# Kernel optimization log

Hardware: AMD Instinct MI355X
Metric: run time of the kernel (lower is better)

Reference implementation:

```python
import jax, jax.numpy as jnp
import numpy as np

B, S, E = 2, 2048, 1024
G, Q, D = 4, 4, 64          # n_groups, queries-per-group, head dim
SCALE = 1.0 / np.sqrt(E).astype(np.float32)  # sequence_attention=False -> 1/sqrt(embed_dim)


def setup_inputs() -> dict:
    key = jax.random.key(0)
    ks = jax.random.split(key, 12)
    init = lambda k, shp, fan_in: jax.random.uniform(k, shp, jnp.float32, -1.0, 1.0) / np.sqrt(fan_in)
    return {
        "q": jax.random.normal(ks[0], (B, S, E), jnp.float32),
        "k": jax.random.normal(ks[1], (B, S, E), jnp.float32),
        "v": jax.random.normal(ks[2], (B, S, E), jnp.float32),
        "Wq_w": init(ks[3], (E, G * Q * D), E),
        "Wq_b": init(ks[4], (G * Q * D,), E),
        "Wk_w": init(ks[5], (E, G * D), E),
        "Wk_b": init(ks[6], (G * D,), E),
        "Wv_w": init(ks[7], (E, G * D), E),
        "Wv_b": init(ks[8], (G * D,), E),
        "fc_w": init(ks[9], (G * Q * D, G * Q * D), G * Q * D),
        "fc_b": init(ks[10], (G * Q * D,), G * Q * D),
    }


def reference(q, k, v, Wq_w, Wq_b, Wk_w, Wk_b, Wv_w, Wv_b, fc_w, fc_b):
    # projections
    qh = (q @ Wq_w + Wq_b).reshape(B, S, G, Q, D)   # b s g q d
    kh = (k @ Wk_w + Wk_b).reshape(B, S, G, D)      # b s g d (1 KV head per group)
    vh = (v @ Wv_w + Wv_b).reshape(B, S, G, D)
    # energy: broadcast single KV head across Q query heads per group
    energy = jnp.einsum('bsgqd,btgd->bgqst', qh, kh) * SCALE  # [b,g,q,s,s]
    attn = jax.nn.softmax(energy, axis=-1)
    out = jnp.einsum('bgqst,btgd->bsgqd', attn, vh)           # b s g q d
    out = out.reshape(B, S, G * Q * D)                        # b s (g q d)
    return out @ fc_w + fc_b
```

## Files before the change

### kernel.cpp

```cpp
#include <hip/hip_runtime.h>


typedef unsigned short u16;
typedef __attribute__((ext_vector_type(4))) unsigned short u16x4;
typedef __attribute__((ext_vector_type(8))) short bf16x8;
typedef __attribute__((ext_vector_type(8))) unsigned short u16x8;
typedef __attribute__((ext_vector_type(4))) float f32x4;
typedef __attribute__((ext_vector_type(8))) float f32x8;

#define MFMA16(a, b, c) __builtin_amdgcn_mfma_f32_16x16x32_bf16(a, b, c, 0, 0, 0)
#define SC2L 0.045084140608f

__device__ __forceinline__ u16 f2b(float f) {
  unsigned int i = __builtin_bit_cast(unsigned int, f);
  i += 0x7fffu + ((i >> 16) & 1u);
  return (u16)(i >> 16);
}
__device__ __forceinline__ unsigned cvtpk_bf16(float a, float b) {
  unsigned r;
  asm("v_cvt_pk_bf16_f32 %0, %1, %2" : "=v"(r) : "v"(a), "v"(b));
  return r;
}
__device__ __forceinline__ void gload_lds16(const u16* g, u16* l) {
  __builtin_amdgcn_global_load_lds(
      (const __attribute__((address_space(1))) unsigned int*)g,
      (__attribute__((address_space(3))) unsigned int*)l, 16, 0, 0);
}

__global__ __launch_bounds__(256) void transpose_all(const float* __restrict__ Wq_w,
                                                     const float* __restrict__ Wk_w,
                                                     const float* __restrict__ Wv_w,
                                                     const float* __restrict__ fc_w,
                                                     u16* __restrict__ WqT,
                                                     u16* __restrict__ WkT,
                                                     u16* __restrict__ WvT,
                                                     u16* __restrict__ fcT) {
  __shared__ u16 tile[32][33];
  int r = blockIdx.x;
  const float* W; u16* Wt; int N; float scale;
  if (r < 1024)      { W = Wq_w; Wt = WqT; N = 1024; scale = SC2L; }
  else if (r < 1280) { W = Wk_w; Wt = WkT; N = 256;  scale = 1.0f; r -= 1024; }
  else if (r < 1536) { W = Wv_w; Wt = WvT; N = 256;  scale = 1.0f; r -= 1280; }
  else               { W = fc_w; Wt = fcT; N = 1024; scale = 1.0f; r -= 1536; }
  const int K = 1024;
  const int bk = (r & 31) * 32;
  const int bn = (r >> 5) * 32;
  const int tx = threadIdx.x & 31, ty = threadIdx.x >> 5;
#pragma unroll
  for (int rr = ty; rr < 32; rr += 8)
    tile[rr][tx] = f2b(W[(size_t)(bk + rr) * N + bn + tx] * scale);
  __syncthreads();
#pragma unroll
  for (int rr = ty; rr < 32; rr += 8) Wt[(size_t)(bn + rr) * K + bk + tx] = tile[tx][rr];
}

template <typename AT, typename CT>
__device__ __forceinline__ void gemm_body(const AT* __restrict__ A,
                                          const u16* __restrict__ Bt,
                                          const float* __restrict__ bias,
                                          CT* __restrict__ C,
                                          int M, int N, int K, float bscale,
                                          bool transv, int bid) {
  __shared__ alignas(16) u16 As[2][64 * 32];
  __shared__ alignas(16) u16 Bs[2][128 * 32];
  const int tid = threadIdx.x;
  const int lane = tid & 63, wave = tid >> 6;
  const int l15 = lane & 15, lg = lane >> 4;
  const int nb = N >> 7;
  const int bm = (bid / nb) << 6;
  const int bn = (bid % nb) << 7;
  const int wr = (wave >> 2) << 5;
  const int wc = (wave & 3) << 5;
  const int crow = tid >> 2;
  const int ccol = (tid & 3) * 8;
  const AT*  arow = A  + (size_t)(bm + crow) * K + ccol;
  const u16* brow = Bt + (size_t)(bn + crow) * K + ccol;

  f32x4 acc[2][2] = {};
  const int nt = K >> 5;

  if (tid < 256) {
    if constexpr (__is_same(AT, float)) {
      const f32x8 af0 = *(const f32x8*)(arow);
      u16x8 av; unsigned* aw = (unsigned*)&av;
#pragma unroll
      for (int j = 0; j < 4; ++j) aw[j] = cvtpk_bf16(af0[2 * j], af0[2 * j + 1]);
      *(u16x8*)(As[0] + tid * 8) = av;
    } else {
      gload_lds16(arow, As[0] + tid * 8);
    }
  }
  gload_lds16(brow, Bs[0] + tid * 8);
  __syncthreads();

#pragma unroll 2
  for (int t = 0; t < nt; ++t) {
    const int c = t & 1;
    const int k1 = (t + 1) << 5;
    f32x8 afn;
    if (t + 1 < nt) {
      if (tid < 256) {
        if constexpr (__is_same(AT, float)) {
          afn = *(const f32x8*)(arow + k1);
        } else {
          gload_lds16(arow + k1, As[c ^ 1] + tid * 8);
        }
      }
      gload_lds16(brow + k1, Bs[c ^ 1] + tid * 8);
    }

    bf16x8 af[2], bf[2];
#pragma unroll
    for (int m = 0; m < 2; ++m)
      af[m] = *(const bf16x8*)(As[c] + (wr + m * 16 + l15) * 32 + lg * 8);
#pragma unroll
    for (int n = 0; n < 2; ++n)
      bf[n] = *(const bf16x8*)(Bs[c] + (wc + n * 16 + l15) * 32 + lg * 8);
#pragma unroll
    for (int m = 0; m < 2; ++m)
#pragma unroll
      for (int n = 0; n < 2; ++n) acc[m][n] = MFMA16(af[m], bf[n], acc[m][n]);

    if constexpr (__is_same(AT, float)) {
      if (t + 1 < nt && tid < 256) {
        u16x8 av; unsigned* aw = (unsigned*)&av;
#pragma unroll
        for (int j = 0; j < 4; ++j) aw[j] = cvtpk_bf16(afn[2 * j], afn[2 * j + 1]);
        *(u16x8*)(As[c ^ 1] + tid * 8) = av;
      }
    }
    __syncthreads();
  }

  float bvv[2];
#pragma unroll
  for (int n = 0; n < 2; ++n) bvv[n] = bias[bn + wc + n * 16 + l15] * bscale;

  if (transv) {
#pragma unroll
    for (int m = 0; m < 2; ++m) {
      const int row = bm + wr + m * 16 + lg * 4;
      const int bb = row >> 11, t = row & 2047;
#pragma unroll
      for (int n = 0; n < 2; ++n) {
        const int col = bn + wc + n * 16 + l15;
        u16x4 pk;
#pragma unroll
        for (int rr = 0; rr < 4; ++rr) pk[rr] = f2b(acc[m][n][rr] + bvv[n]);
        *(u16x4*)(C + (size_t)bb * ((size_t)N * 2048) + (size_t)col * 2048 + t) = pk;
      }
    }
  } else {
#pragma unroll
    for (int m = 0; m < 2; ++m) {
      const int row = bm + wr + m * 16 + lg * 4;
#pragma unroll
      for (int rr = 0; rr < 4; ++rr) {
        CT* cp = C + (size_t)(row + rr) * N + bn + wc + l15;
#pragma unroll
        for (int n = 0; n < 2; ++n) {
          const float val = acc[m][n][rr] + bvv[n];
          if constexpr (__is_same(CT, u16)) cp[n * 16] = f2b(val);
          else                              cp[n * 16] = val;
        }
      }
    }
  }
}

__global__ __launch_bounds__(512, 4) void gemm_qkv(const float* __restrict__ q,
                                                   const float* __restrict__ k,
                                                   const float* __restrict__ v,
                                                   const u16* __restrict__ WqT,
                                                   const u16* __restrict__ WkT,
                                                   const u16* __restrict__ WvT,
                                                   const float* __restrict__ Wq_b,
                                                   const float* __restrict__ Wk_b,
                                                   const float* __restrict__ Wv_b,
                                                   u16* __restrict__ qh,
                                                   u16* __restrict__ kh,
                                                   u16* __restrict__ vt) {
  if (blockIdx.x < 512)
    gemm_body<float, u16>(q, WqT, Wq_b, qh, 4096, 1024, 1024, SC2L, false, blockIdx.x);
  else if (blockIdx.x < 640)
    gemm_body<float, u16>(k, WkT, Wk_b, kh, 4096, 256, 1024, 1.0f, false, blockIdx.x - 512);
  else
    gemm_body<float, u16>(v, WvT, Wv_b, vt, 4096, 256, 1024, 1.0f, true, blockIdx.x - 640);
}

template <typename AT, typename CT, bool TRANSV>
__global__ __launch_bounds__(512, 4) void gemm_bt_bias(const AT* __restrict__ A,
                                                       const u16* __restrict__ Bt,
                                                       const float* __restrict__ bias,
                                                       CT* __restrict__ C,
                                                       int M, int N, int K, float bscale) {
  gemm_body<AT, CT>(A, Bt, bias, C, M, N, K, bscale, TRANSV, blockIdx.x);
}

__global__ __launch_bounds__(512, 2) void attn_fwd(const u16* __restrict__ qh,
                                                   const u16* __restrict__ kh,
                                                   const u16* __restrict__ vhT,
                                                   u16* __restrict__ ao) {
  constexpr int S = 2048;
  __shared__ alignas(16) u16 Klds[2][128][72];
  __shared__ alignas(16) u16 Vt[2][64][136];

  const int tid = threadIdx.x;
  const int lane = tid & 63, w = tid >> 6;
  const int h = w & 3, ssub = w >> 2;
  const int l15 = lane & 15, lg = lane >> 4;
  const int bid = blockIdx.x;
  const int s0 = (bid & 31) << 6;
  const int g = (bid >> 5) & 3;
  const int b = bid >> 7;
  const int sbase = s0 + ssub * 32;

  bf16x8 qf[2][2];
#pragma unroll
  for (int sh = 0; sh < 2; ++sh) {
    const u16* qrow = qh + (((size_t)(b * S + sbase + sh * 16 + l15)) << 10)
                      + g * 256 + h * 64 + lg * 8;
    qf[sh][0] = *(const bf16x8*)(qrow);
    qf[sh][1] = *(const bf16x8*)(qrow + 32);
  }

  const u16* kbase = kh + (((size_t)(b * S)) << 8) + g * 64;
  const u16* vtbase = vhT + ((size_t)(b * 256 + g * 64)) * 2048;

  bf16x8 ones;
#pragma unroll
  for (int j = 0; j < 8; ++j) ones[j] = (short)0x3F80;

  f32x4 lacc[2] = {};
  f32x4 o[2][4] = {};

  const int srow = tid >> 3;
  const int sdp = (tid & 7) * 8;
  const int sig = (srow & 32) | (((srow >> 2) & 1) << 4) | (((srow >> 3) & 3) << 2) | (srow & 3);
  const int vrow = tid >> 4;
  const int vcol = (tid & 15) * 8;

  u16x8 kv[2], vv[2];
#define LOADTILE(T0)                                                                   \
  do {                                                                                 \
    kv[0] = *(const u16x8*)(kbase + (size_t)((T0) + srow) * 256 + sdp);                \
    kv[1] = *(const u16x8*)(kbase + (size_t)((T0) + 64 + srow) * 256 + sdp);           \
    vv[0] = *(const u16x8*)(vtbase + (size_t)vrow * 2048 + (T0) + vcol);               \
    vv[1] = *(const u16x8*)(vtbase + (size_t)(vrow + 32) * 2048 + (T0) + vcol);        \
  } while (0)

  LOADTILE(0);

#pragma unroll 2
  for (int i = 0; i < 16; ++i) {
    const int c = i & 1;
    *(u16x8*)(&Klds[c][sig][sdp])       = kv[0];
    *(u16x8*)(&Klds[c][sig + 64][sdp])  = kv[1];
    *(u16x8*)(&Vt[c][vrow][vcol])       = vv[0];
    *(u16x8*)(&Vt[c][vrow + 32][vcol])  = vv[1];
    __syncthreads();
    if (i + 1 < 16) LOADTILE((i + 1) << 7);

#pragma unroll
    for (int tti = 0; tti < 2; ++tti) {
      const int tt = tti ^ ssub;
#pragma unroll
      for (int kk = 0; kk < 2; ++kk) {
        float p[2][8];
#pragma unroll
        for (int nn = 0; nn < 2; ++nn) {
          const int n = kk * 2 + nn;
          const bf16x8 bk0 = *(const bf16x8*)(&Klds[c][tt * 64 + n * 16 + l15][lg * 8]);
          const bf16x8 bk1 = *(const bf16x8*)(&Klds[c][tt * 64 + n * 16 + l15][32 + lg * 8]);
          __builtin_amdgcn_s_setprio(1);
#pragma unroll
          for (int sh = 0; sh < 2; ++sh) {
            f32x4 z = {};
            z = MFMA16(bk0, qf[sh][0], z);
            z = MFMA16(bk1, qf[sh][1], z);
            __builtin_amdgcn_s_setprio(0);
#pragma unroll
            for (int r = 0; r < 4; ++r)
              p[sh][nn * 4 + r] = exp2f(z[r]);
          }
        }
        bf16x8 pa[2];
#pragma unroll
        for (int sh = 0; sh < 2; ++sh) {
          unsigned* paw = (unsigned*)&pa[sh];
          paw[0] = cvtpk_bf16(p[sh][0], p[sh][1]);
          paw[1] = cvtpk_bf16(p[sh][2], p[sh][3]);
          paw[2] = cvtpk_bf16(p[sh][4], p[sh][5]);
          paw[3] = cvtpk_bf16(p[sh][6], p[sh][7]);
        }
        __builtin_amdgcn_s_setprio(1);
        lacc[0] = MFMA16(pa[0], ones, lacc[0]);
        lacc[1] = MFMA16(pa[1], ones, lacc[1]);
#pragma unroll
        for (int nd = 0; nd < 4; ++nd) {
          const bf16x8 bv = *(const bf16x8*)(&Vt[c][nd * 16 + l15][tt * 64 + kk * 32 + lg * 8]);
          o[0][nd] = MFMA16(pa[0], bv, o[0][nd]);
          o[1][nd] = MFMA16(pa[1], bv, o[1][nd]);
        }
        __builtin_amdgcn_s_setprio(0);
      }
    }
  }
#undef LOADTILE

#pragma unroll
  for (int sh = 0; sh < 2; ++sh) {
#pragma unroll
    for (int r = 0; r < 4; ++r) {
      const float invr = 1.f / lacc[sh][r];
      u16* orow = ao + (((size_t)(b * S + sbase + sh * 16 + lg * 4 + r)) << 10)
                  + g * 256 + h * 64 + l15;
#pragma unroll
      for (int nd = 0; nd < 4; ++nd) orow[nd * 16] = f2b(o[sh][nd][r] * invr);
    }
  }
}

extern "C" void kernel_launch(void* const* d_in, const int* in_sizes, int n_in,
                              void* d_out, int out_size, void* d_ws, size_t ws_size,
                              hipStream_t stream) {
  const float* q    = (const float*)d_in[0];
  const float* k    = (const float*)d_in[1];
  const float* v    = (const float*)d_in[2];
  const float* Wq_w = (const float*)d_in[3];
  const float* Wq_b = (const float*)d_in[4];
  const float* Wk_w = (const float*)d_in[5];
  const float* Wk_b = (const float*)d_in[6];
  const float* Wv_w = (const float*)d_in[7];
  const float* Wv_b = (const float*)d_in[8];
  const float* fc_w = (const float*)d_in[9];
  const float* fc_b = (const float*)d_in[10];
  float* out = (float*)d_out;

  u16* ws  = (u16*)d_ws;
  u16* WqT = ws;
  u16* WkT = WqT + 1024 * 1024;
  u16* WvT = WkT + 256 * 1024;
  u16* fcT = WvT + 256 * 1024;
  u16* qhp = fcT + 1024 * 1024;
  u16* khp = qhp + 4096 * 1024;
  u16* vtp = khp + 4096 * 256;
  u16* aop = vtp + 4096 * 256;

  transpose_all<<<2560, 256, 0, stream>>>(Wq_w, Wk_w, Wv_w, fc_w, WqT, WkT, WvT, fcT);

  gemm_qkv<<<768, 512, 0, stream>>>(q, k, v, WqT, WkT, WvT, Wq_b, Wk_b, Wv_b,
                                    qhp, khp, vtp);

  attn_fwd<<<256, 512, 0, stream>>>(qhp, khp, vtp, aop);

  gemm_bt_bias<u16, float, false><<<512, 512, 0, stream>>>(aop, fcT, fc_b, out, 4096, 1024, 1024, 1.0f);
}
```

Before: 113.8 us.

## Widen GEMM per-wave tiles to 256 threads and double attention KV tile

```diff
diff --git a/kernel.cpp b/kernel.cpp
--- a/kernel.cpp
+++ b/kernel.cpp
@@ -69,28 +69,28 @@
   const int nb = N >> 7;
   const int bm = (bid / nb) << 6;
   const int bn = (bid % nb) << 7;
-  const int wr = (wave >> 2) << 5;
-  const int wc = (wave & 3) << 5;
+  const int wr = (wave >> 1) << 5;
+  const int wc = (wave & 1) << 6;
   const int crow = tid >> 2;
   const int ccol = (tid & 3) * 8;
-  const AT*  arow = A  + (size_t)(bm + crow) * K + ccol;
-  const u16* brow = Bt + (size_t)(bn + crow) * K + ccol;
-
-  f32x4 acc[2][2] = {};
+  const AT*  arow  = A  + (size_t)(bm + crow) * K + ccol;
+  const u16* brow0 = Bt + (size_t)(bn + crow) * K + ccol;
+  const u16* brow1 = Bt + (size_t)(bn + crow + 64) * K + ccol;
+
+  f32x4 acc[2][4] = {};
   const int nt = K >> 5;
 
-  if (tid < 256) {
-    if constexpr (__is_same(AT, float)) {
-      const f32x8 af0 = *(const f32x8*)(arow);
-      u16x8 av; unsigned* aw = (unsigned*)&av;
-#pragma unroll
-      for (int j = 0; j < 4; ++j) aw[j] = cvtpk_bf16(af0[2 * j], af0[2 * j + 1]);
-      *(u16x8*)(As[0] + tid * 8) = av;
-    } else {
-      gload_lds16(arow, As[0] + tid * 8);
-    }
-  }
-  gload_lds16(brow, Bs[0] + tid * 8);
+  if constexpr (__is_same(AT, float)) {
+    const f32x8 af0 = *(const f32x8*)(arow);
+    u16x8 av; unsigned* aw = (unsigned*)&av;
+#pragma unroll
+    for (int j = 0; j < 4; ++j) aw[j] = cvtpk_bf16(af0[2 * j], af0[2 * j + 1]);
+    *(u16x8*)(As[0] + tid * 8) = av;
+  } else {
+    gload_lds16(arow, As[0] + tid * 8);
+  }
+  gload_lds16(brow0, Bs[0] + tid * 8);
+  gload_lds16(brow1, Bs[0] + (tid + 256) * 8);
   __syncthreads();
 
 #pragma unroll 2
@@ -99,30 +99,29 @@
     const int k1 = (t + 1) << 5;
     f32x8 afn;
     if (t + 1 < nt) {
-      if (tid < 256) {
-        if constexpr (__is_same(AT, float)) {
-          afn = *(const f32x8*)(arow + k1);
-        } else {
-          gload_lds16(arow + k1, As[c ^ 1] + tid * 8);
-        }
-      }
-      gload_lds16(brow + k1, Bs[c ^ 1] + tid * 8);
-    }
-
-    bf16x8 af[2], bf[2];
+      if constexpr (__is_same(AT, float)) {
+        afn = *(const f32x8*)(arow + k1);
+      } else {
+        gload_lds16(arow + k1, As[c ^ 1] + tid * 8);
+      }
+      gload_lds16(brow0 + k1, Bs[c ^ 1] + tid * 8);
+      gload_lds16(brow1 + k1, Bs[c ^ 1] + (tid + 256) * 8);
+    }
+
+    bf16x8 af[2], bf[4];
 #pragma unroll
     for (int m = 0; m < 2; ++m)
       af[m] = *(const bf16x8*)(As[c] + (wr + m * 16 + l15) * 32 + lg * 8);
 #pragma unroll
-    for (int n = 0; n < 2; ++n)
+    for (int n = 0; n < 4; ++n)
       bf[n] = *(const bf16x8*)(Bs[c] + (wc + n * 16 + l15) * 32 + lg * 8);
 #pragma unroll
     for (int m = 0; m < 2; ++m)
 #pragma unroll
-      for (int n = 0; n < 2; ++n) acc[m][n] = MFMA16(af[m], bf[n], acc[m][n]);
+      for (int n = 0; n < 4; ++n) acc[m][n] = MFMA16(af[m], bf[n], acc[m][n]);
 
     if constexpr (__is_same(AT, float)) {
-      if (t + 1 < nt && tid < 256) {
+      if (t + 1 < nt) {
         u16x8 av; unsigned* aw = (unsigned*)&av;
 #pragma unroll
         for (int j = 0; j < 4; ++j) aw[j] = cvtpk_bf16(afn[2 * j], afn[2 * j + 1]);
@@ -132,9 +131,9 @@
     __syncthreads();
   }
 
-  float bvv[2];
-#pragma unroll
-  for (int n = 0; n < 2; ++n) bvv[n] = bias[bn + wc + n * 16 + l15] * bscale;
+  float bvv[4];
+#pragma unroll
+  for (int n = 0; n < 4; ++n) bvv[n] = bias[bn + wc + n * 16 + l15] * bscale;
 
   if (transv) {
 #pragma unroll
@@ -142,7 +141,7 @@
       const int row = bm + wr + m * 16 + lg * 4;
       const int bb = row >> 11, t = row & 2047;
 #pragma unroll
-      for (int n = 0; n < 2; ++n) {
+      for (int n = 0; n < 4; ++n) {
         const int col = bn + wc + n * 16 + l15;
         u16x4 pk;
 #pragma unroll
@@ -158,7 +157,7 @@
       for (int rr = 0; rr < 4; ++rr) {
         CT* cp = C + (size_t)(row + rr) * N + bn + wc + l15;
 #pragma unroll
-        for (int n = 0; n < 2; ++n) {
+        for (int n = 0; n < 4; ++n) {
           const float val = acc[m][n][rr] + bvv[n];
           if constexpr (__is_same(CT, u16)) cp[n * 16] = f2b(val);
           else                              cp[n * 16] = val;
@@ -168,7 +167,7 @@
   }
 }
 
-__global__ __launch_bounds__(512, 4) void gemm_qkv(const float* __restrict__ q,
+__global__ __launch_bounds__(256, 4) void gemm_qkv(const float* __restrict__ q,
                                                    const float* __restrict__ k,
                                                    const float* __restrict__ v,
                                                    const u16* __restrict__ WqT,
@@ -189,7 +188,7 @@
 }
 
 template <typename AT, typename CT, bool TRANSV>
-__global__ __launch_bounds__(512, 4) void gemm_bt_bias(const AT* __restrict__ A,
+__global__ __launch_bounds__(256, 4) void gemm_bt_bias(const AT* __restrict__ A,
                                                        const u16* __restrict__ Bt,
                                                        const float* __restrict__ bias,
                                                        CT* __restrict__ C,
@@ -202,8 +201,8 @@
                                                    const u16* __restrict__ vhT,
                                                    u16* __restrict__ ao) {
   constexpr int S = 2048;
-  __shared__ alignas(16) u16 Klds[2][128][72];
-  __shared__ alignas(16) u16 Vt[2][64][136];
+  __shared__ alignas(16) u16 Klds[2][256][72];
+  __shared__ alignas(16) u16 Vt[2][64][264];
 
   const int tid = threadIdx.x;
   const int lane = tid & 63, w = tid >> 6;
@@ -234,36 +233,38 @@
   f32x4 lacc[2] = {};
   f32x4 o[2][4] = {};
 
-  const int srow = tid >> 3;
-  const int sdp = (tid & 7) * 8;
-  const int sig = (srow & 32) | (((srow >> 2) & 1) << 4) | (((srow >> 3) & 3) << 2) | (srow & 3);
-  const int vrow = tid >> 4;
-  const int vcol = (tid & 15) * 8;
-
-  u16x8 kv[2], vv[2];
-#define LOADTILE(T0)                                                                   \
-  do {                                                                                 \
-    kv[0] = *(const u16x8*)(kbase + (size_t)((T0) + srow) * 256 + sdp);                \
-    kv[1] = *(const u16x8*)(kbase + (size_t)((T0) + 64 + srow) * 256 + sdp);           \
-    vv[0] = *(const u16x8*)(vtbase + (size_t)vrow * 2048 + (T0) + vcol);               \
-    vv[1] = *(const u16x8*)(vtbase + (size_t)(vrow + 32) * 2048 + (T0) + vcol);        \
+  const int skrow = tid >> 3;
+  const int skcol = (tid & 7) * 8;
+  const int sigb = (skrow & 32) | (((skrow >> 2) & 1) << 4) | (((skrow >> 3) & 3) << 2) | (skrow & 3);
+  const int svrow = tid >> 5;
+  const int svcol = (tid & 31) * 8;
+
+  u16x8 kvp[4], vvp[4];
+#define LOADTILE(T0)                                                                     \
+  do {                                                                                   \
+    _Pragma("unroll")                                                                    \
+    for (int p = 0; p < 4; ++p) {                                                        \
+      kvp[p] = *(const u16x8*)(kbase + (size_t)((T0) + skrow + 64 * p) * 256 + skcol);   \
+      vvp[p] = *(const u16x8*)(vtbase + (size_t)(svrow + 16 * p) * 2048 + (T0) + svcol); \
+    }                                                                                    \
   } while (0)
 
   LOADTILE(0);
 
 #pragma unroll 2
-  for (int i = 0; i < 16; ++i) {
+  for (int i = 0; i < 8; ++i) {
     const int c = i & 1;
-    *(u16x8*)(&Klds[c][sig][sdp])       = kv[0];
-    *(u16x8*)(&Klds[c][sig + 64][sdp])  = kv[1];
-    *(u16x8*)(&Vt[c][vrow][vcol])       = vv[0];
-    *(u16x8*)(&Vt[c][vrow + 32][vcol])  = vv[1];
+#pragma unroll
+    for (int p = 0; p < 4; ++p) {
+      *(u16x8*)(&Klds[c][sigb + 64 * p][skcol]) = kvp[p];
+      *(u16x8*)(&Vt[c][svrow + 16 * p][svcol])  = vvp[p];
+    }
     __syncthreads();
-    if (i + 1 < 16) LOADTILE((i + 1) << 7);
-
-#pragma unroll
-    for (int tti = 0; tti < 2; ++tti) {
-      const int tt = tti ^ ssub;
+    if (i + 1 < 8) LOADTILE((i + 1) << 8);
+
+#pragma unroll
+    for (int tti = 0; tti < 4; ++tti) {
+      const int tt = (tti + (ssub << 1)) & 3;
 #pragma unroll
       for (int kk = 0; kk < 2; ++kk) {
         float p[2][8];
@@ -349,10 +350,10 @@
 
   transpose_all<<<2560, 256, 0, stream>>>(Wq_w, Wk_w, Wv_w, fc_w, WqT, WkT, WvT, fcT);
 
-  gemm_qkv<<<768, 512, 0, stream>>>(q, k, v, WqT, WkT, WvT, Wq_b, Wk_b, Wv_b,
+  gemm_qkv<<<768, 256, 0, stream>>>(q, k, v, WqT, WkT, WvT, Wq_b, Wk_b, Wv_b,
                                     qhp, khp, vtp);
 
   attn_fwd<<<256, 512, 0, stream>>>(qhp, khp, vtp, aop);
 
-  gemm_bt_bias<u16, float, false><<<512, 512, 0, stream>>>(aop, fcT, fc_b, out, 4096, 1024, 1024, 1.0f);
-}
+  gemm_bt_bias<u16, float, false><<<512, 256, 0, stream>>>(aop, fcT, fc_b, out, 4096, 1024, 1024, 1.0f);
+}
```

Result: slower. 117.4 us (+3.2%).
